# Performance work log

Measured on AMD Instinct MI355X. Metric: run time of the kernel, lower is better.

Reference implementation:

```python
import jax, jax.numpy as jnp
import numpy as np

V, S, D, C = 400000, 4096, 300, 4  # vocab, seq_len, embed_dim, act classes


def setup_inputs() -> dict:
    key = jax.random.key(0)
    ks = jax.random.split(key, 6)
    sc = 1.0 / np.sqrt(D)
    return {
        "x_batch": jax.random.randint(ks[0], (1, S), 0, V),
        "emb_table": jax.random.normal(ks[1], (V, D), jnp.float32) * 0.02,
        "W1": jax.random.normal(ks[2], (D, D), jnp.float32) * sc,
        "b1": jnp.zeros((D,), jnp.float32),
        "Wb": jax.random.normal(ks[3], (D, D), jnp.float32) * sc,  # Bilinear weight [1,D,D] squeezed
        "bb": jnp.zeros((1,), jnp.float32),                        # Bilinear bias
        "W2": jax.random.normal(ks[4], (C, D), jnp.float32) * sc,
        "b2": jnp.zeros((C,), jnp.float32),
    }


def reference(x_batch, emb_table, W1, b1, Wb, bb, W2, b2):
    embed = emb_table[x_batch]                  # [1, S, D] embedding lookup
    dense = embed.mean(axis=1)                  # [1, D] mean pooling
    mid = dense @ W1.T + b1                     # [1, D] hidden layer (dropout = identity in eval)
    # per-token bilinear attention scores: a_s = e_s^T Wb mid + bb (vectorized over s)
    scores = jnp.einsum('sd,de,e->s', embed[0], Wb, mid[0])[None, :] + bb  # [1, S]
    reward = jax.nn.softmax(scores, axis=1)     # [1, S]
    addition = jnp.mean(reward[:, :, None] * embed, axis=1)  # [1, D] weighted mean pooling
    output = (mid + addition) @ W2.T + b2       # [1, C]
    return output, reward
```

## Files before the change

### kernel.cpp

```cpp
#include <hip/hip_runtime.h>
#include <math.h>

#define SEQ  4096
#define DIM  300
#define NCLS 4

#define NB_DENSE 128
#define NB_SC    128
#define NB_ADD   128

#define OFF_P1   0
#define OFF_MID  (OFF_P1 + NB_DENSE * DIM)
#define OFF_U    (OFF_MID + DIM)
#define OFF_SC   (OFF_U + DIM)
#define OFF_BMAX (OFF_SC + SEQ)
#define OFF_P2   (OFF_BMAX + NB_SC)

__global__ __launch_bounds__(256) void k_dense_part(
        const int* __restrict__ x, const float* __restrict__ emb,
        float* __restrict__ p1) {
    __shared__ float lds[4][320];
    const int wave = threadIdx.x >> 6, lane = threadIdx.x & 63;
    float a0 = 0.f, a1 = 0.f, a2 = 0.f, a3 = 0.f, a4 = 0.f;
    const int s0 = blockIdx.x * 32 + wave * 8;
    #pragma unroll
    for (int r = 0; r < 8; ++r) {
        const float* row = emb + (size_t)x[s0 + r] * DIM;
        a0 += row[lane];
        a1 += row[lane + 64];
        a2 += row[lane + 128];
        a3 += row[lane + 192];
        if (lane < DIM - 256) a4 += row[lane + 256];
    }
    lds[wave][lane]       = a0;
    lds[wave][lane + 64]  = a1;
    lds[wave][lane + 128] = a2;
    lds[wave][lane + 192] = a3;
    lds[wave][lane + 256] = a4;
    __syncthreads();
    for (int d = threadIdx.x; d < DIM; d += 256) {
        float s = lds[0][d] + lds[1][d] + lds[2][d] + lds[3][d];
        p1[blockIdx.x * DIM + d] = s;
    }
}

__global__ __launch_bounds__(256) void k_mid(
        const float* __restrict__ p1, const float* __restrict__ W1,
        const float* __restrict__ b1, float* __restrict__ mid) {
    __shared__ float dense[DIM];
    for (int d = threadIdx.x; d < DIM; d += 256) {
        float s = 0.f;
        for (int b = 0; b < NB_DENSE; ++b) s += p1[b * DIM + d];
        dense[d] = s * (1.0f / (float)SEQ);
    }
    __syncthreads();
    const int wave = threadIdx.x >> 6, lane = threadIdx.x & 63;
    const int i = blockIdx.x * 4 + wave;
    const float* w = W1 + (size_t)i * DIM;
    float s = w[lane] * dense[lane] + w[lane + 64] * dense[lane + 64]
            + w[lane + 128] * dense[lane + 128]
            + w[lane + 192] * dense[lane + 192];
    if (lane < DIM - 256) s += w[lane + 256] * dense[lane + 256];
    for (int off = 32; off; off >>= 1) s += __shfl_down(s, off);
    if (lane == 0) mid[i] = s + b1[i];
}

__global__ __launch_bounds__(256) void k_u(
        const float* __restrict__ mid, const float* __restrict__ Wb,
        float* __restrict__ u) {
    __shared__ float v[DIM];
    for (int d = threadIdx.x; d < DIM; d += 256) v[d] = mid[d];
    __syncthreads();
    const int wave = threadIdx.x >> 6, lane = threadIdx.x & 63;
    const int i = blockIdx.x * 4 + wave;
    const float* w = Wb + (size_t)i * DIM;
    float s = w[lane] * v[lane] + w[lane + 64] * v[lane + 64]
            + w[lane + 128] * v[lane + 128] + w[lane + 192] * v[lane + 192];
    if (lane < DIM - 256) s += w[lane + 256] * v[lane + 256];
    for (int off = 32; off; off >>= 1) s += __shfl_down(s, off);
    if (lane == 0) u[i] = s;
}

__global__ __launch_bounds__(256) void k_scores(
        const int* __restrict__ x, const float* __restrict__ emb,
        const float* __restrict__ u, const float* __restrict__ bb,
        float* __restrict__ sc, float* __restrict__ bmax) {
    __shared__ float lmax[4];
    const int wave = threadIdx.x >> 6, lane = threadIdx.x & 63;
    float u0 = u[lane], u1 = u[lane + 64], u2 = u[lane + 128],
          u3 = u[lane + 192];
    float u4 = (lane < DIM - 256) ? u[lane + 256] : 0.f;
    const float bbv = bb[0];
    float wmax = -1e30f;
    const int s0 = blockIdx.x * 32 + wave * 8;
    #pragma unroll
    for (int r = 0; r < 8; ++r) {
        const float* row = emb + (size_t)x[s0 + r] * DIM;
        float s = row[lane] * u0 + row[lane + 64] * u1
                + row[lane + 128] * u2 + row[lane + 192] * u3;
        if (lane < DIM - 256) s += row[lane + 256] * u4;
        for (int off = 32; off; off >>= 1) s += __shfl_down(s, off);
        if (lane == 0) {
            s += bbv;
            sc[s0 + r] = s;
            wmax = fmaxf(wmax, s);
        }
    }
    if (lane == 0) lmax[wave] = wmax;
    __syncthreads();
    if (threadIdx.x == 0)
        bmax[blockIdx.x] =
            fmaxf(fmaxf(lmax[0], lmax[1]), fmaxf(lmax[2], lmax[3]));
}

__global__ __launch_bounds__(256) void k_soft_add(
        const int* __restrict__ x, const float* __restrict__ emb,
        const float* __restrict__ sc, const float* __restrict__ bmax,
        float* __restrict__ reward, float* __restrict__ p2) {
    __shared__ float red[4];
    __shared__ float lds[4][320];
    const int wave = threadIdx.x >> 6, lane = threadIdx.x & 63;
    float m = -1e30f;
    for (int i = threadIdx.x; i < NB_SC; i += 256) m = fmaxf(m, bmax[i]);
    for (int off = 32; off; off >>= 1) m = fmaxf(m, __shfl_down(m, off));
    if (lane == 0) red[wave] = m;
    __syncthreads();
    const float mx = fmaxf(fmaxf(red[0], red[1]), fmaxf(red[2], red[3]));
    __syncthreads();
    float s = 0.f;
    for (int i = threadIdx.x; i < SEQ; i += 256) s += expf(sc[i] - mx);
    for (int off = 32; off; off >>= 1) s += __shfl_down(s, off);
    if (lane == 0) red[wave] = s;
    __syncthreads();
    const float inv = 1.0f / (red[0] + red[1] + red[2] + red[3]);
    float a0 = 0.f, a1 = 0.f, a2 = 0.f, a3 = 0.f, a4 = 0.f;
    const int s0 = blockIdx.x * 32 + wave * 8;
    #pragma unroll
    for (int r = 0; r < 8; ++r) {
        const int srow = s0 + r;
        const float rw = expf(sc[srow] - mx) * inv;
        if (lane == 0) reward[srow] = rw;
        const float* row = emb + (size_t)x[srow] * DIM;
        a0 += rw * row[lane];
        a1 += rw * row[lane + 64];
        a2 += rw * row[lane + 128];
        a3 += rw * row[lane + 192];
        if (lane < DIM - 256) a4 += rw * row[lane + 256];
    }
    lds[wave][lane]       = a0;
    lds[wave][lane + 64]  = a1;
    lds[wave][lane + 128] = a2;
    lds[wave][lane + 192] = a3;
    lds[wave][lane + 256] = a4;
    __syncthreads();
    for (int d = threadIdx.x; d < DIM; d += 256) {
        float t = lds[0][d] + lds[1][d] + lds[2][d] + lds[3][d];
        p2[blockIdx.x * DIM + d] = t;
    }
}

__global__ __launch_bounds__(256) void k_out(
        const float* __restrict__ p2, const float* __restrict__ mid,
        const float* __restrict__ W2, const float* __restrict__ b2,
        float* __restrict__ out) {
    __shared__ float v[DIM];
    for (int d = threadIdx.x; d < DIM; d += 256) {
        float s = 0.f;
        for (int b = 0; b < NB_ADD; ++b) s += p2[b * DIM + d];
        v[d] = mid[d] + s * (1.0f / (float)SEQ);
    }
    __syncthreads();
    const int wave = threadIdx.x >> 6, lane = threadIdx.x & 63;
    const float* w = W2 + (size_t)wave * DIM;
    float s = w[lane] * v[lane] + w[lane + 64] * v[lane + 64]
            + w[lane + 128] * v[lane + 128] + w[lane + 192] * v[lane + 192];
    if (lane < DIM - 256) s += w[lane + 256] * v[lane + 256];
    for (int off = 32; off; off >>= 1) s += __shfl_down(s, off);
    if (lane == 0) out[wave] = s + b2[wave];
}

extern "C" void kernel_launch(void* const* d_in, const int* in_sizes, int n_in,
                              void* d_out, int out_size, void* d_ws,
                              size_t ws_size, hipStream_t stream) {
    const int*   x   = (const int*)d_in[0];
    const float* emb = (const float*)d_in[1];
    const float* W1  = (const float*)d_in[2];
    const float* b1  = (const float*)d_in[3];
    const float* Wb  = (const float*)d_in[4];
    const float* bb  = (const float*)d_in[5];
    const float* W2  = (const float*)d_in[6];
    const float* b2  = (const float*)d_in[7];
    float* out = (float*)d_out;
    float* ws  = (float*)d_ws;

    float* P1   = ws + OFF_P1;
    float* MID  = ws + OFF_MID;
    float* U    = ws + OFF_U;
    float* SC   = ws + OFF_SC;
    float* BMAX = ws + OFF_BMAX;
    float* P2   = ws + OFF_P2;

    k_dense_part<<<NB_DENSE, 256, 0, stream>>>(x, emb, P1);
    k_mid<<<75, 256, 0, stream>>>(P1, W1, b1, MID);
    k_u<<<75, 256, 0, stream>>>(MID, Wb, U);
    k_scores<<<NB_SC, 256, 0, stream>>>(x, emb, U, bb, SC, BMAX);
    k_soft_add<<<NB_ADD, 256, 0, stream>>>(x, emb, SC, BMAX, out + NCLS, P2);
    k_out<<<1, 256, 0, stream>>>(P2, MID, W2, b2, out);
}
```

Baseline: 566.7 us.

## Fuse six-kernel pipeline into one cooperative kernel with grid syncs

Merges the six separate kernels (dense partials, mid matvec, Wb matvec, scores, softmax+weighted sum, output) into one cooperative kernel of 128 blocks, with grid.sync() between stages. This removes the per-launch overhead and the inter-kernel gaps of six dependent launches. In exchange it adds grid-wide barrier costs and relies on cooperative launch support. Blocks idle during the 75-block matvec stages and the single-block output stage.

```diff
diff --git a/kernel.cpp b/kernel.cpp
--- a/kernel.cpp
+++ b/kernel.cpp
@@ -1,182 +1,180 @@
 #include <hip/hip_runtime.h>
+#include <hip/hip_cooperative_groups.h>
 #include <math.h>
+
+namespace cg = cooperative_groups;
 
 #define SEQ  4096
 #define DIM  300
 #define NCLS 4
-
-#define NB_DENSE 128
-#define NB_SC    128
-#define NB_ADD   128
+#define NB   128
 
 #define OFF_P1   0
-#define OFF_MID  (OFF_P1 + NB_DENSE * DIM)
+#define OFF_MID  (OFF_P1 + NB * DIM)
 #define OFF_U    (OFF_MID + DIM)
 #define OFF_SC   (OFF_U + DIM)
 #define OFF_BMAX (OFF_SC + SEQ)
-#define OFF_P2   (OFF_BMAX + NB_SC)
+#define OFF_P2   (OFF_BMAX + NB)
 
-__global__ __launch_bounds__(256) void k_dense_part(
+__global__ __launch_bounds__(256) void fused_dan(
         const int* __restrict__ x, const float* __restrict__ emb,
-        float* __restrict__ p1) {
+        const float* __restrict__ W1, const float* __restrict__ b1,
+        const float* __restrict__ Wb, const float* __restrict__ bb,
+        const float* __restrict__ W2, const float* __restrict__ b2,
+        float* __restrict__ out, float* __restrict__ ws) {
+    cg::grid_group grid = cg::this_grid();
+
+    float* P1     = ws + OFF_P1;
+    float* MID    = ws + OFF_MID;
+    float* U      = ws + OFF_U;
+    float* SC     = ws + OFF_SC;
+    float* BMAX   = ws + OFF_BMAX;
+    float* P2     = ws + OFF_P2;
+    float* reward = out + NCLS;
+
     __shared__ float lds[4][320];
+    __shared__ float vec[DIM];
+    __shared__ float red[4];
+
     const int wave = threadIdx.x >> 6, lane = threadIdx.x & 63;
-    float a0 = 0.f, a1 = 0.f, a2 = 0.f, a3 = 0.f, a4 = 0.f;
-    const int s0 = blockIdx.x * 32 + wave * 8;
-    #pragma unroll
-    for (int r = 0; r < 8; ++r) {
-        const float* row = emb + (size_t)x[s0 + r] * DIM;
-        a0 += row[lane];
-        a1 += row[lane + 64];
-        a2 += row[lane + 128];
-        a3 += row[lane + 192];
-        if (lane < DIM - 256) a4 += row[lane + 256];
+    const int bid  = blockIdx.x;
+    const int s0   = bid * 32 + wave * 8;
+
+    {
+        float a0 = 0.f, a1 = 0.f, a2 = 0.f, a3 = 0.f, a4 = 0.f;
+        #pragma unroll
+        for (int r = 0; r < 8; ++r) {
+            const float* row = emb + (size_t)x[s0 + r] * DIM;
+            a0 += row[lane];
+            a1 += row[lane + 64];
+            a2 += row[lane + 128];
+            a3 += row[lane + 192];
+            if (lane < DIM - 256) a4 += row[lane + 256];
+        }
+        lds[wave][lane]       = a0;
+        lds[wave][lane + 64]  = a1;
+        lds[wave][lane + 128] = a2;
+        lds[wave][lane + 192] = a3;
+        lds[wave][lane + 256] = a4;
+        __syncthreads();
+        for (int d = threadIdx.x; d < DIM; d += 256)
+            P1[bid * DIM + d] = lds[0][d] + lds[1][d] + lds[2][d] + lds[3][d];
     }
-    lds[wave][lane]       = a0;
-    lds[wave][lane + 64]  = a1;
-    lds[wave][lane + 128] = a2;
-    lds[wave][lane + 192] = a3;
-    lds[wave][lane + 256] = a4;
-    __syncthreads();
-    for (int d = threadIdx.x; d < DIM; d += 256) {
-        float s = lds[0][d] + lds[1][d] + lds[2][d] + lds[3][d];
-        p1[blockIdx.x * DIM + d] = s;
+    grid.sync();
+
+    if (bid < 75) {
+        for (int d = threadIdx.x; d < DIM; d += 256) {
+            float s = 0.f;
+            for (int b = 0; b < NB; ++b) s += P1[b * DIM + d];
+            vec[d] = s * (1.0f / (float)SEQ);
+        }
+        __syncthreads();
+        const int i    = bid * 4 + wave;
+        const float* w = W1 + (size_t)i * DIM;
+        float s = w[lane] * vec[lane] + w[lane + 64] * vec[lane + 64]
+                + w[lane + 128] * vec[lane + 128]
+                + w[lane + 192] * vec[lane + 192];
+        if (lane < DIM - 256) s += w[lane + 256] * vec[lane + 256];
+        for (int off = 32; off; off >>= 1) s += __shfl_down(s, off);
+        if (lane == 0) MID[i] = s + b1[i];
     }
-}
+    grid.sync();
 
-__global__ __launch_bounds__(256) void k_mid(
-        const float* __restrict__ p1, const float* __restrict__ W1,
-        const float* __restrict__ b1, float* __restrict__ mid) {
-    __shared__ float dense[DIM];
-    for (int d = threadIdx.x; d < DIM; d += 256) {
+    if (bid < 75) {
+        for (int d = threadIdx.x; d < DIM; d += 256) vec[d] = MID[d];
+        __syncthreads();
+        const int i    = bid * 4 + wave;
+        const float* w = Wb + (size_t)i * DIM;
+        float s = w[lane] * vec[lane] + w[lane + 64] * vec[lane + 64]
+                + w[lane + 128] * vec[lane + 128]
+                + w[lane + 192] * vec[lane + 192];
+        if (lane < DIM - 256) s += w[lane + 256] * vec[lane + 256];
+        for (int off = 32; off; off >>= 1) s += __shfl_down(s, off);
+        if (lane == 0) U[i] = s;
+    }
+    grid.sync();
+
+    {
+        const float u0 = U[lane], u1 = U[lane + 64], u2 = U[lane + 128],
+                    u3 = U[lane + 192];
+        const float u4  = (lane < DIM - 256) ? U[lane + 256] : 0.f;
+        const float bbv = bb[0];
+        float wmax = -1e30f;
+        #pragma unroll
+        for (int r = 0; r < 8; ++r) {
+            const float* row = emb + (size_t)x[s0 + r] * DIM;
+            float s = row[lane] * u0 + row[lane + 64] * u1
+                    + row[lane + 128] * u2 + row[lane + 192] * u3;
+            if (lane < DIM - 256) s += row[lane + 256] * u4;
+            for (int off = 32; off; off >>= 1) s += __shfl_down(s, off);
+            if (lane == 0) {
+                s += bbv;
+                SC[s0 + r] = s;
+                wmax = fmaxf(wmax, s);
+            }
+        }
+        if (lane == 0) red[wave] = wmax;
+        __syncthreads();
+        if (threadIdx.x == 0)
+            BMAX[bid] =
+                fmaxf(fmaxf(red[0], red[1]), fmaxf(red[2], red[3]));
+    }
+    grid.sync();
+
+    {
+        float m = -1e30f;
+        for (int i = threadIdx.x; i < NB; i += 256) m = fmaxf(m, BMAX[i]);
+        for (int off = 32; off; off >>= 1) m = fmaxf(m, __shfl_down(m, off));
+        if (lane == 0) red[wave] = m;
+        __syncthreads();
+        const float mx = fmaxf(fmaxf(red[0], red[1]), fmaxf(red[2], red[3]));
+        __syncthreads();
         float s = 0.f;
-        for (int b = 0; b < NB_DENSE; ++b) s += p1[b * DIM + d];
-        dense[d] = s * (1.0f / (float)SEQ);
+        for (int i = threadIdx.x; i < SEQ; i += 256) s += expf(SC[i] - mx);
+        for (int off = 32; off; off >>= 1) s += __shfl_down(s, off);
+        if (lane == 0) red[wave] = s;
+        __syncthreads();
+        const float inv = 1.0f / (red[0] + red[1] + red[2] + red[3]);
+
+        float a0 = 0.f, a1 = 0.f, a2 = 0.f, a3 = 0.f, a4 = 0.f;
+        #pragma unroll
+        for (int r = 0; r < 8; ++r) {
+            const int srow = s0 + r;
+            const float rw = expf(SC[srow] - mx) * inv;
+            if (lane == 0) reward[srow] = rw;
+            const float* row = emb + (size_t)x[srow] * DIM;
+            a0 += rw * row[lane];
+            a1 += rw * row[lane + 64];
+            a2 += rw * row[lane + 128];
+            a3 += rw * row[lane + 192];
+            if (lane < DIM - 256) a4 += rw * row[lane + 256];
+        }
+        lds[wave][lane]       = a0;
+        lds[wave][lane + 64]  = a1;
+        lds[wave][lane + 128] = a2;
+        lds[wave][lane + 192] = a3;
+        lds[wave][lane + 256] = a4;
+        __syncthreads();
+        for (int d = threadIdx.x; d < DIM; d += 256)
+            P2[bid * DIM + d] = lds[0][d] + lds[1][d] + lds[2][d] + lds[3][d];
     }
-    __syncthreads();
-    const int wave = threadIdx.x >> 6, lane = threadIdx.x & 63;
-    const int i = blockIdx.x * 4 + wave;
-    const float* w = W1 + (size_t)i * DIM;
-    float s = w[lane] * dense[lane] + w[lane + 64] * dense[lane + 64]
-            + w[lane + 128] * dense[lane + 128]
-            + w[lane + 192] * dense[lane + 192];
-    if (lane < DIM - 256) s += w[lane + 256] * dense[lane + 256];
-    for (int off = 32; off; off >>= 1) s += __shfl_down(s, off);
-    if (lane == 0) mid[i] = s + b1[i];
-}
+    grid.sync();
 
-__global__ __launch_bounds__(256) void k_u(
-        const float* __restrict__ mid, const float* __restrict__ Wb,
-        float* __restrict__ u) {
-    __shared__ float v[DIM];
-    for (int d = threadIdx.x; d < DIM; d += 256) v[d] = mid[d];
-    __syncthreads();
-    const int wave = threadIdx.x >> 6, lane = threadIdx.x & 63;
-    const int i = blockIdx.x * 4 + wave;
-    const float* w = Wb + (size_t)i * DIM;
-    float s = w[lane] * v[lane] + w[lane + 64] * v[lane + 64]
-            + w[lane + 128] * v[lane + 128] + w[lane + 192] * v[lane + 192];
-    if (lane < DIM - 256) s += w[lane + 256] * v[lane + 256];
-    for (int off = 32; off; off >>= 1) s += __shfl_down(s, off);
-    if (lane == 0) u[i] = s;
-}
-
-__global__ __launch_bounds__(256) void k_scores(
-        const int* __restrict__ x, const float* __restrict__ emb,
-        const float* __restrict__ u, const float* __restrict__ bb,
-        float* __restrict__ sc, float* __restrict__ bmax) {
-    __shared__ float lmax[4];
-    const int wave = threadIdx.x >> 6, lane = threadIdx.x & 63;
-    float u0 = u[lane], u1 = u[lane + 64], u2 = u[lane + 128],
-          u3 = u[lane + 192];
-    float u4 = (lane < DIM - 256) ? u[lane + 256] : 0.f;
-    const float bbv = bb[0];
-    float wmax = -1e30f;
-    const int s0 = blockIdx.x * 32 + wave * 8;
-    #pragma unroll
-    for (int r = 0; r < 8; ++r) {
-        const float* row = emb + (size_t)x[s0 + r] * DIM;
-        float s = row[lane] * u0 + row[lane + 64] * u1
-                + row[lane + 128] * u2 + row[lane + 192] * u3;
-        if (lane < DIM - 256) s += row[lane + 256] * u4;
+    if (bid == 0) {
+        for (int d = threadIdx.x; d < DIM; d += 256) {
+            float s = 0.f;
+            for (int b = 0; b < NB; ++b) s += P2[b * DIM + d];
+            vec[d] = MID[d] + s * (1.0f / (float)SEQ);
+        }
+        __syncthreads();
+        const float* w = W2 + (size_t)wave * DIM;
+        float s = w[lane] * vec[lane] + w[lane + 64] * vec[lane + 64]
+                + w[lane + 128] * vec[lane + 128]
+                + w[lane + 192] * vec[lane + 192];
+        if (lane < DIM - 256) s += w[lane + 256] * vec[lane + 256];
         for (int off = 32; off; off >>= 1) s += __shfl_down(s, off);
-        if (lane == 0) {
-            s += bbv;
-            sc[s0 + r] = s;
-            wmax = fmaxf(wmax, s);
-        }
+        if (lane == 0) out[wave] = s + b2[wave];
     }
-    if (lane == 0) lmax[wave] = wmax;
-    __syncthreads();
-    if (threadIdx.x == 0)
-        bmax[blockIdx.x] =
-            fmaxf(fmaxf(lmax[0], lmax[1]), fmaxf(lmax[2], lmax[3]));
-}
-
-__global__ __launch_bounds__(256) void k_soft_add(
-        const int* __restrict__ x, const float* __restrict__ emb,
-        const float* __restrict__ sc, const float* __restrict__ bmax,
-        float* __restrict__ reward, float* __restrict__ p2) {
-    __shared__ float red[4];
-    __shared__ float lds[4][320];
-    const int wave = threadIdx.x >> 6, lane = threadIdx.x & 63;
-    float m = -1e30f;
-    for (int i = threadIdx.x; i < NB_SC; i += 256) m = fmaxf(m, bmax[i]);
-    for (int off = 32; off; off >>= 1) m = fmaxf(m, __shfl_down(m, off));
-    if (lane == 0) red[wave] = m;
-    __syncthreads();
-    const float mx = fmaxf(fmaxf(red[0], red[1]), fmaxf(red[2], red[3]));
-    __syncthreads();
-    float s = 0.f;
-    for (int i = threadIdx.x; i < SEQ; i += 256) s += expf(sc[i] - mx);
-    for (int off = 32; off; off >>= 1) s += __shfl_down(s, off);
-    if (lane == 0) red[wave] = s;
-    __syncthreads();
-    const float inv = 1.0f / (red[0] + red[1] + red[2] + red[3]);
-    float a0 = 0.f, a1 = 0.f, a2 = 0.f, a3 = 0.f, a4 = 0.f;
-    const int s0 = blockIdx.x * 32 + wave * 8;
-    #pragma unroll
-    for (int r = 0; r < 8; ++r) {
-        const int srow = s0 + r;
-        const float rw = expf(sc[srow] - mx) * inv;
-        if (lane == 0) reward[srow] = rw;
-        const float* row = emb + (size_t)x[srow] * DIM;
-        a0 += rw * row[lane];
-        a1 += rw * row[lane + 64];
-        a2 += rw * row[lane + 128];
-        a3 += rw * row[lane + 192];
-        if (lane < DIM - 256) a4 += rw * row[lane + 256];
-    }
-    lds[wave][lane]       = a0;
-    lds[wave][lane + 64]  = a1;
-    lds[wave][lane + 128] = a2;
-    lds[wave][lane + 192] = a3;
-    lds[wave][lane + 256] = a4;
-    __syncthreads();
-    for (int d = threadIdx.x; d < DIM; d += 256) {
-        float t = lds[0][d] + lds[1][d] + lds[2][d] + lds[3][d];
-        p2[blockIdx.x * DIM + d] = t;
-    }
-}
-
-__global__ __launch_bounds__(256) void k_out(
-        const float* __restrict__ p2, const float* __restrict__ mid,
-        const float* __restrict__ W2, const float* __restrict__ b2,
-        float* __restrict__ out) {
-    __shared__ float v[DIM];
-    for (int d = threadIdx.x; d < DIM; d += 256) {
-        float s = 0.f;
-        for (int b = 0; b < NB_ADD; ++b) s += p2[b * DIM + d];
-        v[d] = mid[d] + s * (1.0f / (float)SEQ);
-    }
-    __syncthreads();
-    const int wave = threadIdx.x >> 6, lane = threadIdx.x & 63;
-    const float* w = W2 + (size_t)wave * DIM;
-    float s = w[lane] * v[lane] + w[lane + 64] * v[lane + 64]
-            + w[lane + 128] * v[lane + 128] + w[lane + 192] * v[lane + 192];
-    if (lane < DIM - 256) s += w[lane + 256] * v[lane + 256];
-    for (int off = 32; off; off >>= 1) s += __shfl_down(s, off);
-    if (lane == 0) out[wave] = s + b2[wave];
 }
 
 extern "C" void kernel_launch(void* const* d_in, const int* in_sizes, int n_in,
@@ -193,17 +191,9 @@
     float* out = (float*)d_out;
     float* ws  = (float*)d_ws;
 
-    float* P1   = ws + OFF_P1;
-    float* MID  = ws + OFF_MID;
-    float* U    = ws + OFF_U;
-    float* SC   = ws + OFF_SC;
-    float* BMAX = ws + OFF_BMAX;
-    float* P2   = ws + OFF_P2;
-
-    k_dense_part<<<NB_DENSE, 256, 0, stream>>>(x, emb, P1);
-    k_mid<<<75, 256, 0, stream>>>(P1, W1, b1, MID);
-    k_u<<<75, 256, 0, stream>>>(MID, Wb, U);
-    k_scores<<<NB_SC, 256, 0, stream>>>(x, emb, U, bb, SC, BMAX);
-    k_soft_add<<<NB_ADD, 256, 0, stream>>>(x, emb, SC, BMAX, out + NCLS, P2);
-    k_out<<<1, 256, 0, stream>>>(P2, MID, W2, b2, out);
+    void* args[] = {(void*)&x,  (void*)&emb, (void*)&W1, (void*)&b1,
+                    (void*)&Wb, (void*)&bb,  (void*)&W2, (void*)&b2,
+                    (void*)&out, (void*)&ws};
+    hipLaunchCooperativeKernel((void*)fused_dan, dim3(NB), dim3(256), args, 0,
+                               stream);
 }
```

New measurement: 651.4 us. +14.9%, slower.
